# Optimization experiments

Hardware: AMD Instinct MI355X
Metric: run time of the kernel (lower is better)

The kernel has to match this reference:

```python
import jax, jax.numpy as jnp
import numpy as np

D = 256      # n_feature
LVL = 17     # tree depth (leaf levels)
MIX = 20     # M mixture components


def _lstm_cell(x, h, c, Wih, Whh, bih, bhh):
    # torch.nn.LSTMCell gate order: i, f, g, o
    g = x @ Wih.T + bih + h @ Whh.T + bhh
    i, f, gg, o = jnp.split(g, 4, axis=1)
    c2 = jax.nn.sigmoid(f) * c + jax.nn.sigmoid(i) * jnp.tanh(gg)
    return jax.nn.sigmoid(o) * jnp.tanh(c2), c2


def _get_parameter(y, M):
    parts = jnp.split(y[:, :13 * M], 13, axis=1)
    pi = jax.nn.softmax(parts[0], axis=1)
    mu_x, mu_y = parts[1], parts[2]
    sx, sy = jnp.exp(parts[3]), jnp.exp(parts[4])
    rho_xy = jnp.tanh(parts[5])
    mu_a, mu_b = parts[6], parts[7]
    sa, sb = jnp.exp(parts[8]), jnp.exp(parts[9])
    rho_ab = jnp.tanh(parts[10])
    mu_s, ss = parts[11], jnp.exp(parts[12])
    q = jax.nn.softmax(y[:, -3:], axis=1)
    return (pi, mu_x, mu_y, sx, sy, rho_xy, mu_a, mu_b, sa, sb, rho_ab, mu_s, ss, q)


def _bvn_logpdf(dx, dy, mx, my, sx, sy, rho):
    zx = (dx - mx) / sx
    zy = (dy - my) / sy
    Z = zx ** 2 + zy ** 2 - 2.0 * rho * zx * zy
    return -Z / (2.0 * (1.0 - rho ** 2)) - jnp.log(2.0 * jnp.pi * sx * sy * jnp.sqrt(1.0 - rho ** 2))


def _nll(pt, prm):
    # pt: [n, 8] = (x, y, a, b, slope, p1, p2, p3); prm: GMM parameters, each [n, M]
    pi, mx, my, sx, sy, rxy, ma, mb, sa, sb, rab, ms, ss, q = prm
    lpi = jnp.log(pi)
    dx, dy, da, db, ds = (pt[:, k:k + 1] for k in range(5))
    p = pt[:, 5:8]
    lse = jax.scipy.special.logsumexp
    lxy = lse(lpi + _bvn_logpdf(dx, dy, mx, my, sx, sy, rxy), axis=1)
    lab = lse(lpi + _bvn_logpdf(da, db, ma, mb, sa, sb, rab), axis=1)
    lsl = lse(lpi - (ds - ms) ** 2 / (2.0 * ss ** 2) - jnp.log(jnp.sqrt(2.0 * jnp.pi) * ss), axis=1)
    pen = -(p * jnp.log(q)).sum(axis=1)
    return -(lxy + lab + lsl) + pen


def _expected_pos(prm):
    pi, mx, my, sx, sy, rxy, ma, mb, sa, sb, rab, ms, ss, q = prm
    e = lambda m: (pi * m).sum(axis=1)
    return jnp.concatenate([jnp.stack([e(mx), e(my), e(ma), e(mb), e(ms)], axis=1), q], axis=1)


def _levels(I_flat):
    # I_flat is bottom-up concatenation of per-level [ni,3] blocks of a full binary tree
    n_int = I_flat.shape[0]
    L = int(np.log2(n_int + 1))
    sizes = [2 ** (L - 1 - i) for i in range(L)]
    offs = np.concatenate([[0], np.cumsum(sizes)])
    return [I_flat[offs[i]:offs[i + 1]] for i in range(L)]


def setup_inputs() -> dict:
    key = jax.random.key(0)
    ks = jax.random.split(key, 16)
    N = 2 ** (LVL + 1) - 1  # 262143 total nodes
    # heap-layout full binary tree: children of i are 2i+1, 2i+2; bottom-up levels
    blocks = []
    for l in range(LVL - 1, -1, -1):
        f = np.arange(2 ** l - 1, 2 ** (l + 1) - 1)
        blocks.append(np.stack([2 * f + 1, 2 * f + 2, f], axis=1))
    I_flat = jnp.asarray(np.concatenate(blocks, 0), dtype=jnp.int32)
    s = 0.05
    return {
        "X": jax.random.normal(ks[0], (N, 8), jnp.float32),
        "Feature": jax.random.normal(ks[1], (N, D), jnp.float32),
        "I_flat": I_flat,
        "W_ih_e": jax.random.normal(ks[2], (4 * (D // 2), 8), jnp.float32) * s,
        "W_hh_e": jax.random.normal(ks[3], (4 * (D // 2), D // 2), jnp.float32) * s,
        "b_ih_e": jax.random.normal(ks[4], (4 * (D // 2),), jnp.float32) * s,
        "b_hh_e": jax.random.normal(ks[5], (4 * (D // 2),), jnp.float32) * s,
        "fc_h_W": jax.random.normal(ks[6], (2 * D, D), jnp.float32) * s,
        "fc_h_b": jax.random.normal(ks[7], (2 * D,), jnp.float32) * s,
        "W_ih_d": jax.random.normal(ks[8], (4 * D, D + 8), jnp.float32) * s,
        "W_hh_d": jax.random.normal(ks[9], (4 * D, D), jnp.float32) * s,
        "b_ih_d": jax.random.normal(ks[10], (4 * D,), jnp.float32) * s,
        "b_hh_d": jax.random.normal(ks[11], (4 * D,), jnp.float32) * s,
        "fc_W": jax.random.normal(ks[12], (13 * MIX + 3, D // 2), jnp.float32) * s,
        "fc_b": jax.random.normal(ks[13], (13 * MIX + 3,), jnp.float32) * s,
    }


def reference(X, Feature, I_flat, W_ih_e, W_hh_e, b_ih_e, b_hh_e,
              fc_h_W, fc_h_b, W_ih_d, W_hh_d, b_ih_d, b_hh_d, fc_W, fc_b):
    levels = _levels(I_flat)
    num_I = len(levels)

    # ---- encode: bottom-up gather children -> LSTMCell -> scatter father ----
    Feature_New = Feature
    for I in levels:
        li, ri, fi = I[:, 0], I[:, 1], I[:, 2]
        hl, cl = jnp.split(Feature[li], 2, axis=1)
        hr, cr = jnp.split(Feature[ri], 2, axis=1)
        hlo, clo = _lstm_cell(X[li], hl, cl, W_ih_e, W_hh_e, b_ih_e, b_hh_e)
        hro, cro = _lstm_cell(X[ri], hr, cr, W_ih_e, W_hh_e, b_ih_e, b_hh_e)
        out = jnp.concatenate([hlo + hro, clo + cro], axis=1)
        Feature_New = Feature_New.at[fi].set(out)

    # ---- decode: top-down gather father -> LSTMCell+GMM head -> scatter children ----
    X_P = X
    Feat = Feature_New
    Loss = jnp.float32(0.0)
    for I in reversed(levels):
        li, ri, fi = I[:, 0], I[:, 1], I[:, 2]
        p_l, p_r, p_f = X[li], X[ri], X[fi]
        f_f = Feat[fi]
        z = jnp.tanh(f_f @ fc_h_W.T + fc_h_b)
        h_f, c_f = jnp.split(z, 2, axis=1)
        h_o, c_o = _lstm_cell(jnp.concatenate([p_f, f_f], axis=1), h_f, c_f,
                              W_ih_d, W_hh_d, b_ih_d, b_hh_d)
        h_left, h_right = jnp.split(h_o, 2, axis=1)
        c_left, c_right = jnp.split(c_o, 2, axis=1)
        prm_l = _get_parameter(h_left @ fc_W.T + fc_b, MIX)
        prm_r = _get_parameter(h_right @ fc_W.T + fc_b, MIX)
        direct = _nll(p_l, prm_l) + _nll(p_r, prm_r)
        swapped = _nll(p_l, prm_r) + _nll(p_r, prm_l)
        sw = swapped < direct  # l_r_index == 1 -> swap left/right outputs
        Loss = Loss + jnp.mean(jnp.where(sw, swapped, direct))
        pos_l, pos_r = _expected_pos(prm_l), _expected_pos(prm_r)
        feat_l = jnp.concatenate([h_left, c_left], axis=1)
        feat_r = jnp.concatenate([h_right, c_right], axis=1)
        swc = sw[:, None]
        Feat = Feat.at[li].set(jnp.where(swc, feat_r, feat_l))
        Feat = Feat.at[ri].set(jnp.where(swc, feat_l, feat_r))
        X_P = X_P.at[li].set(jnp.where(swc, pos_r, pos_l))
        X_P = X_P.at[ri].set(jnp.where(swc, pos_l, pos_r))
    return Loss / num_I
```

## Files before the change

### kernel.cpp

```cpp
#include <hip/hip_runtime.h>
#include <hip/hip_bf16.h>
#include <math.h>


#define LOG2PI 1.8378770664093453f

typedef __attribute__((ext_vector_type(8))) short short8;
typedef __attribute__((ext_vector_type(4))) float f32x4;

__device__ inline float frcp(float x) { return __builtin_amdgcn_rcpf(x); }
__device__ inline float fexp(float x) { return __expf(x); }
__device__ inline float flog(float x) { return __logf(x); }
__device__ inline float ftanh(float x) {
    float xc = fminf(fmaxf(x, -10.f), 10.f);
    float e = __expf(2.f * xc);
    return (e - 1.f) * frcp(e + 1.f);
}
__device__ inline float sigm(float x) {
    float xc = fminf(fmaxf(x, -30.f), 30.f);
    return frcp(1.f + __expf(-xc));
}

__device__ inline ushort f2b(float v) {
    union { float f; unsigned u; } x; x.f = v;
    unsigned r = x.u + 0x7fffu + ((x.u >> 16) & 1u);
    return (ushort)(r >> 16);
}
__device__ inline float b2f(ushort h) {
    union { unsigned u; float f; } x; x.u = ((unsigned)h) << 16; return x.f;
}

__device__ inline void gload16(const void* g, void* l) {
    __builtin_amdgcn_global_load_lds(
        (const __attribute__((address_space(1))) unsigned*)g,
        (__attribute__((address_space(3))) unsigned*)l, 16, 0, 0);
}

__device__ inline f32x4 mfma16(short8 a, short8 b, f32x4 c) {
    return __builtin_amdgcn_mfma_f32_16x16x32_bf16(a, b, c, 0, 0, 0);
}

__device__ inline float halfmax(float v) {
    #pragma unroll
    for (int o = 16; o >= 1; o >>= 1) v = fmaxf(v, __shfl_xor(v, o));
    return v;
}
__device__ inline float halfsum(float v) {
    #pragma unroll
    for (int o = 16; o >= 1; o >>= 1) v += __shfl_xor(v, o);
    return v;
}
__device__ inline float lse20(float t) {
    float m = halfmax(t);
    float s = halfsum(fexp(t - m));
    return m + flog(s);
}

__device__ inline float nll_node(const ushort* yb, const float* X,
                                 long long fi, int lane, bool& sw_out)
{
    const int half = lane >> 5, k = lane & 31;
    float v = (k < 20) ? b2f(yb[k]) : -INFINITY;
    float mm = halfmax(v);
    float se = halfsum((k < 20) ? fexp(v - mm) : 0.f);
    float lpi = v - mm - flog(se);
    float mx = 0, my = 0, rsx = 1, rsy = 1, rho = 0, hro = 0, cxy = 0;
    float ma = 0, mb2 = 0, rsa = 1, rsb = 1, rab = 0, hra = 0, cab = 0;
    float ms = 0, hrs = 0, csl = 0;
    if (k < 20) {
        mx = b2f(yb[20 + k]); my = b2f(yb[40 + k]);
        float lsx = b2f(yb[60 + k]), lsy = b2f(yb[80 + k]);
        rsx = fexp(-lsx); rsy = fexp(-lsy);
        rho = ftanh(b2f(yb[100 + k]));
        float omr = 1.f - rho * rho;
        hro = 0.5f * frcp(omr);
        cxy = LOG2PI + lsx + lsy + 0.5f * flog(omr);
        ma = b2f(yb[120 + k]); mb2 = b2f(yb[140 + k]);
        float lsa = b2f(yb[160 + k]), lsb = b2f(yb[180 + k]);
        rsa = fexp(-lsa); rsb = fexp(-lsb);
        rab = ftanh(b2f(yb[200 + k]));
        float omr2 = 1.f - rab * rab;
        hra = 0.5f * frcp(omr2);
        cab = LOG2PI + lsa + lsb + 0.5f * flog(omr2);
        ms = b2f(yb[220 + k]); float lss = b2f(yb[240 + k]);
        float rss = fexp(-lss);
        hrs = 0.5f * rss * rss;
        csl = 0.5f * LOG2PI + lss;
    }
    float lq0, lq1, lq2;
    {
        float q0 = b2f(yb[260]), q1 = b2f(yb[261]), q2 = b2f(yb[262]);
        float qm = fmaxf(q0, fmaxf(q1, q2));
        float l = flog(fexp(q0 - qm) + fexp(q1 - qm) + fexp(q2 - qm)) + qm;
        lq0 = q0 - l; lq1 = q1 - l; lq2 = q2 - l;
    }
    const float* pl = X + (size_t)(2 * fi + 1) * 8;
    const float* pr = X + (size_t)(2 * fi + 2) * 8;
    float res[2];
    #pragma unroll
    for (int s = 0; s < 2; ++s) {
        const float* pt = s ? pr : pl;
        float dx = pt[0], dy = pt[1], da = pt[2], db = pt[3], ds = pt[4];
        float t1 = -INFINITY, t2 = -INFINITY, t3 = -INFINITY;
        if (k < 20) {
            float zx = (dx - mx) * rsx, zy = (dy - my) * rsy;
            float Zz = zx * zx + zy * zy - 2.f * rho * zx * zy;
            t1 = lpi - Zz * hro - cxy;
            float za = (da - ma) * rsa, zb = (db - mb2) * rsb;
            float Z2 = za * za + zb * zb - 2.f * rab * za * zb;
            t2 = lpi - Z2 * hra - cab;
            float zs = ds - ms;
            t3 = lpi - zs * zs * hrs - csl;
        }
        float l1 = lse20(t1), l2 = lse20(t2), l3 = lse20(t3);
        float pen = -(pt[5] * lq0 + pt[6] * lq1 + pt[7] * lq2);
        res[s] = -(l1 + l2 + l3) + pen;
    }
    float Aval = half ? res[1] : res[0];
    float Bval = half ? res[0] : res[1];
    float direct = Aval + __shfl_xor(Aval, 32);
    float swapped = Bval + __shfl_xor(Bval, 32);
    sw_out = swapped < direct;
    return sw_out ? swapped : direct;
}

__device__ inline void feat_write_ap(ushort* Ap, const ushort* Hj,
                                     const ushort* Cj, long long fi, bool sw,
                                     int lane)
{
    const size_t rowL = 2 * (size_t)fi + 1;
    const int offL = sw ? 128 : 0;
    const int offR = 128 - offL;
    const int part = lane >> 5;
    const int c = (lane & 31) * 4;
    ushort4 vL = *(const ushort4*)((part ? Cj : Hj) + offL + c);
    ushort4 vR = *(const ushort4*)((part ? Cj : Hj) + offR + c);
    *(ushort4*)(Ap + rowL * 576 + 8 + part * 128 + c) = vL;
    *(ushort4*)(Ap + (rowL + 1) * 576 + 8 + part * 128 + c) = vR;
}

__global__ __launch_bounds__(256) void z_gemm(
    ushort* __restrict__ Apc,
    const ushort* __restrict__ Wz,
    const float* __restrict__ fc_h_b,
    ushort* __restrict__ Zcc,
    int M)
{
    __shared__ ushort As[128 * 64];
    __shared__ ushort Bs[128 * 64];
    const int tid = threadIdx.x;
    const int lane = tid & 63;
    const int w = tid >> 6;
    const int wr = w >> 1, wc = w & 1;
    const int fr = lane & 15, fq = lane >> 4;
    const int m0 = blockIdx.x * 128, n0 = blockIdx.y * 128;

    f32x4 acc[4][4] = {};

    #pragma unroll
    for (int k0 = 0; k0 < 256; k0 += 64) {
        __syncthreads();
        #pragma unroll
        for (int it = 0; it < 4; ++it) {
            const int i = it * 256 + tid;
            const int row = i >> 3, slot = i & 7;
            const int sl = slot ^ (row & 7);
            const int wbase = (i - lane) * 8;
            {
                int gm = m0 + row; gm = gm < M ? gm : M - 1;
                gload16(Apc + (size_t)gm * 576 + 8 + k0 + sl * 8, &As[wbase]);
            }
            {
                int gn = n0 + row; gn = gn < 512 ? gn : 511;
                gload16(Wz + (size_t)gn * 256 + k0 + sl * 8, &Bs[wbase]);
            }
        }
        __syncthreads();
        #pragma unroll
        for (int ks = 0; ks < 2; ++ks) {
            short8 af[4], bfr[4];
            #pragma unroll
            for (int mr = 0; mr < 4; ++mr) {
                const int row = wr * 64 + mr * 16 + fr;
                const int sl = (ks * 4 + fq) ^ (row & 7);
                af[mr] = *(const short8*)&As[row * 64 + sl * 8];
            }
            #pragma unroll
            for (int nc = 0; nc < 4; ++nc) {
                const int row = wc * 64 + nc * 16 + fr;
                const int sl = (ks * 4 + fq) ^ (row & 7);
                bfr[nc] = *(const short8*)&Bs[row * 64 + sl * 8];
            }
            #pragma unroll
            for (int mr = 0; mr < 4; ++mr)
                #pragma unroll
                for (int nc = 0; nc < 4; ++nc)
                    acc[mr][nc] = mfma16(af[mr], bfr[nc], acc[mr][nc]);
        }
    }

    #pragma unroll
    for (int mr = 0; mr < 4; ++mr) {
        #pragma unroll
        for (int j = 0; j < 4; ++j) {
            const int row = m0 + wr * 64 + mr * 16 + fq * 4 + j;
            if (row >= M) continue;
            #pragma unroll
            for (int nc = 0; nc < 4; ++nc) {
                const int col = n0 + wc * 64 + nc * 16 + fr;
                const float z = ftanh(acc[mr][nc][j] + fc_h_b[col]);
                if (col < 256)
                    Apc[(size_t)row * 576 + 264 + col] = f2b(z);
                else
                    Zcc[(size_t)row * 256 + (col - 256)] = f2b(z);
            }
        }
    }
}

__global__ __launch_bounds__(256) void gates_lstm(
    const ushort* __restrict__ Apc,
    const ushort* __restrict__ Wg,
    const float*  __restrict__ bg,
    const ushort* __restrict__ Zcc,
    ushort* __restrict__ H, ushort* __restrict__ C, int M)
{
    __shared__ ushort As[128 * 64];
    __shared__ ushort Bs[128 * 64];
    const int tid = threadIdx.x;
    const int lane = tid & 63;
    const int w = tid >> 6;
    const int wr = w >> 1, wc = w & 1;
    const int fr = lane & 15, fq = lane >> 4;
    const int m0 = blockIdx.x * 128, n0 = blockIdx.y * 128;

    f32x4 acc[4][4] = {};

    #pragma unroll
    for (int k0 = 0; k0 < 576; k0 += 64) {
        __syncthreads();
        #pragma unroll
        for (int it = 0; it < 4; ++it) {
            const int i = it * 256 + tid;
            const int row = i >> 3, slot = i & 7;
            const int sl = slot ^ (row & 7);
            const int wbase = (i - lane) * 8;
            {
                int gm = m0 + row; gm = gm < M ? gm : M - 1;
                gload16(Apc + (size_t)gm * 576 + k0 + sl * 8, &As[wbase]);
            }
            gload16(Wg + (size_t)(n0 + row) * 576 + k0 + sl * 8, &Bs[wbase]);
        }
        __syncthreads();
        #pragma unroll
        for (int ks = 0; ks < 2; ++ks) {
            short8 af[4], bfr[4];
            #pragma unroll
            for (int mr = 0; mr < 4; ++mr) {
                const int row = wr * 64 + mr * 16 + fr;
                const int sl = (ks * 4 + fq) ^ (row & 7);
                af[mr] = *(const short8*)&As[row * 64 + sl * 8];
            }
            #pragma unroll
            for (int nc = 0; nc < 4; ++nc) {
                const int row = wc * 64 + nc * 16 + fr;
                const int sl = (ks * 4 + fq) ^ (row & 7);
                bfr[nc] = *(const short8*)&Bs[row * 64 + sl * 8];
            }
            #pragma unroll
            for (int mr = 0; mr < 4; ++mr)
                #pragma unroll
                for (int nc = 0; nc < 4; ++nc)
                    acc[mr][nc] = mfma16(af[mr], bfr[nc], acc[mr][nc]);
        }
    }

    const int q = fr & 3;
    #pragma unroll
    for (int mr = 0; mr < 4; ++mr) {
        const int node = m0 + wr * 64 + mr * 16 + fq * 4 + q;
        #pragma unroll
        for (int nc = 0; nc < 4; ++nc) {
            const int col = n0 + wc * 64 + nc * 16 + fr;
            f32x4 v = acc[mr][nc];
            const float b = bg[col];
            v[0] += b; v[1] += b; v[2] += b; v[3] += b;
            float gv[4];
            gv[q] = v[q];
            #pragma unroll
            for (int m = 1; m < 4; ++m)
                gv[q ^ m] = __shfl_xor(v[q ^ m], m);
            if (node < M) {
                const int t = (col >> 2) & 255;
                const float cf = b2f(Zcc[(size_t)node * 256 + t]);
                const float c2 = sigm(gv[1]) * cf + sigm(gv[0]) * ftanh(gv[2]);
                const float hv = sigm(gv[3]) * ftanh(c2);
                H[(size_t)node * 256 + t] = f2b(hv);
                C[(size_t)node * 256 + t] = f2b(c2);
            }
        }
    }
}

#define YS 272
__global__ __launch_bounds__(256) void ynll_z(
    const ushort* __restrict__ Hb, const ushort* __restrict__ Cc,
    const ushort* __restrict__ Wyp,
    const float* __restrict__ fc_b, const float* __restrict__ X,
    ushort* __restrict__ Ap,
    const ushort* __restrict__ Wz, const float* __restrict__ fc_h_b,
    ushort* __restrict__ Zcc,
    float* __restrict__ loss,
    int Bc, long long nb_fi, float scale, int writeFeat)
{
    __shared__ char pool[17408] __attribute__((aligned(16)));
    __shared__ float lsum[4];
    ushort* Hs  = (ushort*)pool;
    ushort* Ysb = (ushort*)pool;
    ushort* Fs  = (ushort*)pool;
    const int tid = threadIdx.x;
    const int lane = tid & 63;
    const int wv = tid >> 6;
    const int fr = lane & 15, fq = lane >> 4;
    const int n16 = blockIdx.x * 16;

    #pragma unroll
    for (int it = 0; it < 2; ++it) {
        const int i = it * 256 + tid;
        const int row = i >> 4, slot = i & 15;
        const int sl = slot ^ (row & 7);
        int gr = n16 * 2 + row;
        const int grmax = 2 * Bc - 1;
        gr = gr <= grmax ? gr : grmax;
        gload16(Hb + (size_t)gr * 128 + sl * 8, &Hs[(i - lane) * 8]);
    }
    __syncthreads();

    f32x4 acc[2][5] = {};
    #pragma unroll
    for (int ks = 0; ks < 4; ++ks) {
        short8 a[2];
        #pragma unroll
        for (int rf = 0; rf < 2; ++rf) {
            const int row = rf * 16 + fr;
            const int sl = (ks * 4 + fq) ^ (row & 7);
            a[rf] = *(const short8*)&Hs[row * 128 + sl * 8];
        }
        #pragma unroll
        for (int n = 0; n < 5; ++n) {
            const short8 b = *(const short8*)(
                Wyp + (size_t)(wv * 80 + n * 16 + fr) * 128 + ks * 32 + fq * 8);
            acc[0][n] = mfma16(a[0], b, acc[0][n]);
            acc[1][n] = mfma16(a[1], b, acc[1][n]);
        }
    }
    __syncthreads();

    #pragma unroll
    for (int rf = 0; rf < 2; ++rf)
        #pragma unroll
        for (int n = 0; n < 5; ++n)
            #pragma unroll
            for (int j = 0; j < 4; ++j) {
                const int row = rf * 16 + fq * 4 + j;
                const int col = wv * 80 + n * 16 + fr;
                if (col < 263)
                    Ysb[row * YS + col] = f2b(acc[rf][n][j] + fc_b[col]);
            }
    __syncthreads();

    float wsum = 0.f;
    #pragma unroll
    for (int s4 = 0; s4 < 4; ++s4) {
        const int jj = wv * 4 + s4;
        const int j = n16 + jj;
        if (j >= Bc) break;
        bool sw;
        const long long fi = nb_fi + j;
        wsum += nll_node(&Ysb[(2 * jj + (lane >> 5)) * YS], X, fi, lane, sw);
        if (writeFeat)
            feat_write_ap(Ap, Hb + (size_t)j * 256, Cc + (size_t)j * 256,
                          fi, sw, lane);
    }
    if (lane == 0) lsum[wv] = wsum;
    __syncthreads();
    if (tid == 0)
        atomicAdd(loss, (lsum[0] + lsum[1] + lsum[2] + lsum[3]) * scale);

    if (!writeFeat) return;

    const size_t base = 2 * (size_t)(nb_fi + n16) + 1;
    const int rmax = 2 * Bc - 2 * n16 - 1;
    #pragma unroll
    for (int it = 0; it < 4; ++it) {
        const int i = it * 256 + tid;
        const int row = i >> 5, slot = i & 31;
        const int sl = slot ^ (row & 7);
        int r = row; r = r <= rmax ? r : rmax;
        gload16(Ap + (base + r) * 576 + 8 + sl * 8, &Fs[(i - lane) * 8]);
    }
    __syncthreads();

    f32x4 zacc[2][8] = {};
    for (int ks = 0; ks < 8; ++ks) {
        short8 a[2];
        #pragma unroll
        for (int mf = 0; mf < 2; ++mf) {
            const int r = mf * 16 + fr;
            const int ss = (ks * 4 + fq) ^ (r & 7);
            a[mf] = *(const short8*)&Fs[r * 256 + ss * 8];
        }
        #pragma unroll
        for (int nf = 0; nf < 8; ++nf) {
            const short8 b = *(const short8*)(
                Wz + (size_t)(wv * 128 + nf * 16 + fr) * 256 + ks * 32 + fq * 8);
            zacc[0][nf] = mfma16(a[0], b, zacc[0][nf]);
            zacc[1][nf] = mfma16(a[1], b, zacc[1][nf]);
        }
    }
    #pragma unroll
    for (int mf = 0; mf < 2; ++mf)
        #pragma unroll
        for (int nf = 0; nf < 8; ++nf)
            #pragma unroll
            for (int j = 0; j < 4; ++j) {
                const int r = mf * 16 + fq * 4 + j;
                if (r > rmax) continue;
                const int col = wv * 128 + nf * 16 + fr;
                const float z = ftanh(zacc[mf][nf][j] + fc_h_b[col]);
                if (col < 256)
                    Ap[(base + r) * 576 + 264 + col] = f2b(z);
                else
                    Zcc[(size_t)(2 * n16 + r) * 256 + (col - 256)] = f2b(z);
            }
}

__global__ __launch_bounds__(256) void pack_all(
    const float* __restrict__ fc_h_W, ushort* __restrict__ Wz,
    const float* __restrict__ Wih, const float* __restrict__ Whh,
    ushort* __restrict__ Wg,
    const float* __restrict__ bih, const float* __restrict__ bhh,
    float* __restrict__ bg,
    const float* __restrict__ fcW, ushort* __restrict__ Wy,
    const float* __restrict__ X, ushort* __restrict__ Ap, int nInt)
{
    int i = blockIdx.x * 256 + threadIdx.x;
    if (i < 131072) { Wz[i] = f2b(fc_h_W[i]); return; }
    i -= 131072;
    if (i < 589824) {
        int np = i / 576, c = i - np * 576;
        int n = (np & 3) * 256 + (np >> 2);
        float v = 0.f;
        if (c < 264) v = Wih[n * 264 + c];
        else if (c < 520) v = Whh[n * 256 + (c - 264)];
        Wg[i] = f2b(v);
        return;
    }
    i -= 589824;
    if (i < 1024) {
        int n = (i & 3) * 256 + (i >> 2);
        bg[i] = bih[n] + bhh[n];
        return;
    }
    i -= 1024;
    if (i < 40960) {
        int r = i / 128;
        Wy[i] = f2b(r < 263 ? fcW[i] : 0.f);
        return;
    }
    i -= 40960;
    if (i < nInt * 8) {
        int row = i >> 3, s = i & 7;
        if (s == 0) {
            const float* xs = X + (size_t)row * 8;
            short8 v;
            #pragma unroll
            for (int k = 0; k < 8; ++k)
                ((ushort*)&v)[k] = f2b(xs[k]);
            *(short8*)(Ap + (size_t)row * 576) = v;
        } else {
            short8 z = {0, 0, 0, 0, 0, 0, 0, 0};
            *(short8*)(Ap + (size_t)row * 576 + (64 + s) * 8) = z;
        }
    }
}

__global__ __launch_bounds__(256) void encoder_root(
    const float* __restrict__ X, const float* __restrict__ Feature,
    const float* __restrict__ Wih, const float* __restrict__ Whh,
    const float* __restrict__ bih, const float* __restrict__ bhh,
    ushort* __restrict__ Ap)
{
    __shared__ float gsh[2][512];
    __shared__ float hc[2][256];
    const int t = threadIdx.x;
    for (int ch = 0; ch < 2; ++ch) {
        const int node = 1 + ch;
        const float* x = X + node * 8;
        const float* h = Feature + (size_t)node * 256;
        #pragma unroll
        for (int gi = 0; gi < 2; ++gi) {
            int g = t + gi * 256;
            float s = bih[g] + bhh[g];
            const float* wi = Wih + (size_t)g * 8;
            #pragma unroll
            for (int k = 0; k < 8; ++k) s += wi[k] * x[k];
            const float* wh = Whh + (size_t)g * 128;
            for (int k = 0; k < 128; ++k) s += wh[k] * h[k];
            gsh[ch][g] = s;
        }
    }
    __syncthreads();
    {
        int ch = t >> 7, u = t & 127;
        float i_ = gsh[ch][u], f_ = gsh[ch][128 + u];
        float gg = gsh[ch][256 + u], o_ = gsh[ch][384 + u];
        float c = Feature[(size_t)(1 + ch) * 256 + 128 + u];
        float c2 = sigm(f_) * c + sigm(i_) * ftanh(gg);
        hc[ch][u] = sigm(o_) * ftanh(c2);
        hc[ch][128 + u] = c2;
    }
    __syncthreads();
    Ap[8 + t] = f2b(hc[0][t] + hc[1][t]);
}

extern "C" void kernel_launch(void* const* d_in, const int* in_sizes, int n_in,
                              void* d_out, int out_size, void* d_ws, size_t ws_size,
                              hipStream_t stream)
{
    const float* X       = (const float*)d_in[0];
    const float* Feature = (const float*)d_in[1];
    const float* W_ih_e  = (const float*)d_in[3];
    const float* W_hh_e  = (const float*)d_in[4];
    const float* b_ih_e  = (const float*)d_in[5];
    const float* b_hh_e  = (const float*)d_in[6];
    const float* fc_h_W  = (const float*)d_in[7];
    const float* fc_h_b  = (const float*)d_in[8];
    const float* W_ih_d  = (const float*)d_in[9];
    const float* W_hh_d  = (const float*)d_in[10];
    const float* b_ih_d  = (const float*)d_in[11];
    const float* b_hh_d  = (const float*)d_in[12];
    const float* fc_W    = (const float*)d_in[13];
    const float* fc_b    = (const float*)d_in[14];
    const int Nnodes = in_sizes[0] / 8;
    const int nInt = (Nnodes - 1) / 2;

    float* out = (float*)d_out;
    hipMemsetAsync(d_out, 0, sizeof(float), stream);

    char* cur = (char*)d_ws;
    auto take = [&](size_t bytes) {
        char* p = cur;
        cur += (bytes + 255) & ~(size_t)255;
        return p;
    };
    ushort* Ap  = (ushort*)take((size_t)(nInt + 1) * 576 * 2);
    ushort* Wz  = (ushort*)take((size_t)512 * 256 * 2);
    ushort* Wg  = (ushort*)take((size_t)1024 * 576 * 2);
    ushort* Wy  = (ushort*)take((size_t)320 * 128 * 2);
    float*  bg  = (float*) take((size_t)1024 * 4);
    ushort* Zcc = (ushort*)take((size_t)65536 * 256 * 2);
    ushort* Hb  = (ushort*)take((size_t)65536 * 256 * 2);
    ushort* Cc  = (ushort*)take((size_t)65536 * 256 * 2);

    const int packTotal = 131072 + 589824 + 1024 + 40960 + nInt * 8;
    pack_all<<<(packTotal + 255) / 256, 256, 0, stream>>>(
        fc_h_W, Wz, W_ih_d, W_hh_d, Wg, b_ih_d, b_hh_d, bg, fc_W, Wy,
        X, Ap, nInt);

    encoder_root<<<1, 256, 0, stream>>>(X, Feature, W_ih_e, W_hh_e,
                                        b_ih_e, b_hh_e, Ap);

    z_gemm<<<dim3(1, 4), 256, 0, stream>>>(Ap, Wz, fc_h_b, Zcc, 1);

    for (int l = 0; l < 17; ++l) {
        const int B = 1 << l;
        const long long nb = B - 1;
        const int writeFeat = (l < 16) ? 1 : 0;
        const float scale = 1.f / ((float)B * 17.f);
        const int mg = (B + 127) / 128;
        gates_lstm<<<dim3(mg, 8), 256, 0, stream>>>(
            Ap + (size_t)nb * 576, Wg, bg, Zcc, Hb, Cc, B);
        ynll_z<<<(B + 15) / 16, 256, 0, stream>>>(
            Hb, Cc, Wy, fc_b, X, Ap, Wz, fc_h_b, Zcc, out,
            B, nb, scale, writeFeat);
    }
}
```

Measured before the change: 1.383 ms.

## Split z-projection GEMM out of ynll into a separate per-level z_gemm launch

Removes the fused fc_h projection (Z = tanh(F Wz^T + b)) from the tail of the NLL kernel and instead launches the standalone z_gemm kernel at the start of each level over the level's nodes. The fused version ran a small 32-row MFMA tile per 16-node block, re-reading Wz from global for each block. The standalone GEMM can use larger tiles with better weight reuse. In exchange it adds one kernel launch per level and a global round-trip of the features between kernels.

```diff
diff --git a/kernel.cpp b/kernel.cpp
--- a/kernel.cpp
+++ b/kernel.cpp
@@ -303,21 +303,17 @@
 }
 
 #define YS 272
-__global__ __launch_bounds__(256) void ynll_z(
+__global__ __launch_bounds__(256) void ynll(
     const ushort* __restrict__ Hb, const ushort* __restrict__ Cc,
     const ushort* __restrict__ Wyp,
     const float* __restrict__ fc_b, const float* __restrict__ X,
-    ushort* __restrict__ Ap,
-    const ushort* __restrict__ Wz, const float* __restrict__ fc_h_b,
-    ushort* __restrict__ Zcc,
-    float* __restrict__ loss,
+    ushort* __restrict__ Ap, float* __restrict__ loss,
     int Bc, long long nb_fi, float scale, int writeFeat)
 {
     __shared__ char pool[17408] __attribute__((aligned(16)));
     __shared__ float lsum[4];
     ushort* Hs  = (ushort*)pool;
     ushort* Ysb = (ushort*)pool;
-    ushort* Fs  = (ushort*)pool;
     const int tid = threadIdx.x;
     const int lane = tid & 63;
     const int wv = tid >> 6;
@@ -386,53 +382,6 @@
     __syncthreads();
     if (tid == 0)
         atomicAdd(loss, (lsum[0] + lsum[1] + lsum[2] + lsum[3]) * scale);
-
-    if (!writeFeat) return;
-
-    const size_t base = 2 * (size_t)(nb_fi + n16) + 1;
-    const int rmax = 2 * Bc - 2 * n16 - 1;
-    #pragma unroll
-    for (int it = 0; it < 4; ++it) {
-        const int i = it * 256 + tid;
-        const int row = i >> 5, slot = i & 31;
-        const int sl = slot ^ (row & 7);
-        int r = row; r = r <= rmax ? r : rmax;
-        gload16(Ap + (base + r) * 576 + 8 + sl * 8, &Fs[(i - lane) * 8]);
-    }
-    __syncthreads();
-
-    f32x4 zacc[2][8] = {};
-    for (int ks = 0; ks < 8; ++ks) {
-        short8 a[2];
-        #pragma unroll
-        for (int mf = 0; mf < 2; ++mf) {
-            const int r = mf * 16 + fr;
-            const int ss = (ks * 4 + fq) ^ (r & 7);
-            a[mf] = *(const short8*)&Fs[r * 256 + ss * 8];
-        }
-        #pragma unroll
-        for (int nf = 0; nf < 8; ++nf) {
-            const short8 b = *(const short8*)(
-                Wz + (size_t)(wv * 128 + nf * 16 + fr) * 256 + ks * 32 + fq * 8);
-            zacc[0][nf] = mfma16(a[0], b, zacc[0][nf]);
-            zacc[1][nf] = mfma16(a[1], b, zacc[1][nf]);
-        }
-    }
-    #pragma unroll
-    for (int mf = 0; mf < 2; ++mf)
-        #pragma unroll
-        for (int nf = 0; nf < 8; ++nf)
-            #pragma unroll
-            for (int j = 0; j < 4; ++j) {
-                const int r = mf * 16 + fq * 4 + j;
-                if (r > rmax) continue;
-                const int col = wv * 128 + nf * 16 + fr;
-                const float z = ftanh(zacc[mf][nf][j] + fc_h_b[col]);
-                if (col < 256)
-                    Ap[(base + r) * 576 + 264 + col] = f2b(z);
-                else
-                    Zcc[(size_t)(2 * n16 + r) * 256 + (col - 256)] = f2b(z);
-            }
 }
 
 __global__ __launch_bounds__(256) void pack_all(
@@ -571,18 +520,18 @@
     encoder_root<<<1, 256, 0, stream>>>(X, Feature, W_ih_e, W_hh_e,
                                         b_ih_e, b_hh_e, Ap);
 
-    z_gemm<<<dim3(1, 4), 256, 0, stream>>>(Ap, Wz, fc_h_b, Zcc, 1);
-
     for (int l = 0; l < 17; ++l) {
         const int B = 1 << l;
         const long long nb = B - 1;
         const int writeFeat = (l < 16) ? 1 : 0;
         const float scale = 1.f / ((float)B * 17.f);
         const int mg = (B + 127) / 128;
+        ushort* Apc = Ap + (size_t)nb * 576;
+        z_gemm<<<dim3(mg, 4), 256, 0, stream>>>(Apc, Wz, fc_h_b, Zcc, B);
         gates_lstm<<<dim3(mg, 8), 256, 0, stream>>>(
-            Ap + (size_t)nb * 576, Wg, bg, Zcc, Hb, Cc, B);
-        ynll_z<<<(B + 15) / 16, 256, 0, stream>>>(
-            Hb, Cc, Wy, fc_b, X, Ap, Wz, fc_h_b, Zcc, out,
+            Apc, Wg, bg, Zcc, Hb, Cc, B);
+        ynll<<<(B + 15) / 16, 256, 0, stream>>>(
+            Hb, Cc, Wy, fc_b, X, Ap, out,
             B, nb, scale, writeFeat);
     }
 }
```

Measured after the change: 1.231 ms. -11.0%, faster.

## Split fused NLL/Z kernel at deep levels and source features from H/C

Applied to the files above, without the earlier changes.

The fused NLL+Z kernel is split by tree level. Shallow levels (l<=10) keep a fused variant that reads child features directly from Hb/Cc using swap flags in shared memory, rather than re-reading them from Ap after writing. Deeper levels use a separate NLL kernel followed by a wide z_gemm launch, which gets better parallelism and weight reuse than 16-row blocks. The encoder root computation is folded into block 0 of pack_all to save a launch. The cost is an extra kernel launch per deep level.

```diff
diff --git a/kernel.cpp b/kernel.cpp
--- a/kernel.cpp
+++ b/kernel.cpp
@@ -303,21 +303,17 @@
 }
 
 #define YS 272
-__global__ __launch_bounds__(256) void ynll_z(
+__global__ __launch_bounds__(256) void ynll(
     const ushort* __restrict__ Hb, const ushort* __restrict__ Cc,
     const ushort* __restrict__ Wyp,
     const float* __restrict__ fc_b, const float* __restrict__ X,
-    ushort* __restrict__ Ap,
-    const ushort* __restrict__ Wz, const float* __restrict__ fc_h_b,
-    ushort* __restrict__ Zcc,
-    float* __restrict__ loss,
+    ushort* __restrict__ Ap, float* __restrict__ loss,
     int Bc, long long nb_fi, float scale, int writeFeat)
 {
     __shared__ char pool[17408] __attribute__((aligned(16)));
     __shared__ float lsum[4];
     ushort* Hs  = (ushort*)pool;
     ushort* Ysb = (ushort*)pool;
-    ushort* Fs  = (ushort*)pool;
     const int tid = threadIdx.x;
     const int lane = tid & 63;
     const int wv = tid >> 6;
@@ -386,10 +382,93 @@
     __syncthreads();
     if (tid == 0)
         atomicAdd(loss, (lsum[0] + lsum[1] + lsum[2] + lsum[3]) * scale);
-
-    if (!writeFeat) return;
-
-    const size_t base = 2 * (size_t)(nb_fi + n16) + 1;
+}
+
+__global__ __launch_bounds__(256) void ynll_zs(
+    const ushort* __restrict__ Hb, const ushort* __restrict__ Cc,
+    const ushort* __restrict__ Wyp,
+    const float* __restrict__ fc_b, const float* __restrict__ X,
+    ushort* __restrict__ Ap,
+    const ushort* __restrict__ Wz, const float* __restrict__ fc_h_b,
+    ushort* __restrict__ Zcc,
+    float* __restrict__ loss,
+    int Bc, long long nb_fi, float scale)
+{
+    __shared__ char pool[17408] __attribute__((aligned(16)));
+    __shared__ float lsum[4];
+    __shared__ int sw_sh[16];
+    ushort* Hs  = (ushort*)pool;
+    ushort* Ysb = (ushort*)pool;
+    ushort* Fs  = (ushort*)pool;
+    const int tid = threadIdx.x;
+    const int lane = tid & 63;
+    const int wv = tid >> 6;
+    const int fr = lane & 15, fq = lane >> 4;
+    const int n16 = blockIdx.x * 16;
+
+    #pragma unroll
+    for (int it = 0; it < 2; ++it) {
+        const int i = it * 256 + tid;
+        const int row = i >> 4, slot = i & 15;
+        const int sl = slot ^ (row & 7);
+        int gr = n16 * 2 + row;
+        const int grmax = 2 * Bc - 1;
+        gr = gr <= grmax ? gr : grmax;
+        gload16(Hb + (size_t)gr * 128 + sl * 8, &Hs[(i - lane) * 8]);
+    }
+    __syncthreads();
+
+    f32x4 acc[2][5] = {};
+    #pragma unroll
+    for (int ks = 0; ks < 4; ++ks) {
+        short8 a[2];
+        #pragma unroll
+        for (int rf = 0; rf < 2; ++rf) {
+            const int row = rf * 16 + fr;
+            const int sl = (ks * 4 + fq) ^ (row & 7);
+            a[rf] = *(const short8*)&Hs[row * 128 + sl * 8];
+        }
+        #pragma unroll
+        for (int n = 0; n < 5; ++n) {
+            const short8 b = *(const short8*)(
+                Wyp + (size_t)(wv * 80 + n * 16 + fr) * 128 + ks * 32 + fq * 8);
+            acc[0][n] = mfma16(a[0], b, acc[0][n]);
+            acc[1][n] = mfma16(a[1], b, acc[1][n]);
+        }
+    }
+    __syncthreads();
+
+    #pragma unroll
+    for (int rf = 0; rf < 2; ++rf)
+        #pragma unroll
+        for (int n = 0; n < 5; ++n)
+            #pragma unroll
+            for (int j = 0; j < 4; ++j) {
+                const int row = rf * 16 + fq * 4 + j;
+                const int col = wv * 80 + n * 16 + fr;
+                if (col < 263)
+                    Ysb[row * YS + col] = f2b(acc[rf][n][j] + fc_b[col]);
+            }
+    __syncthreads();
+
+    float wsum = 0.f;
+    #pragma unroll
+    for (int s4 = 0; s4 < 4; ++s4) {
+        const int jj = wv * 4 + s4;
+        const int j = n16 + jj;
+        if (j >= Bc) break;
+        bool sw;
+        const long long fi = nb_fi + j;
+        wsum += nll_node(&Ysb[(2 * jj + (lane >> 5)) * YS], X, fi, lane, sw);
+        if (lane == 0) sw_sh[jj] = sw ? 1 : 0;
+        feat_write_ap(Ap, Hb + (size_t)j * 256, Cc + (size_t)j * 256,
+                      fi, sw, lane);
+    }
+    if (lane == 0) lsum[wv] = wsum;
+    __syncthreads();
+    if (tid == 0)
+        atomicAdd(loss, (lsum[0] + lsum[1] + lsum[2] + lsum[3]) * scale);
+
     const int rmax = 2 * Bc - 2 * n16 - 1;
     #pragma unroll
     for (int it = 0; it < 4; ++it) {
@@ -397,7 +476,14 @@
         const int row = i >> 5, slot = i & 31;
         const int sl = slot ^ (row & 7);
         int r = row; r = r <= rmax ? r : rmax;
-        gload16(Ap + (base + r) * 576 + 8 + sl * 8, &Fs[(i - lane) * 8]);
+        const int pj = r >> 1, side = r & 1;
+        const int sw = sw_sh[pj];
+        const int off = side ? (sw ? 0 : 128) : (sw ? 128 : 0);
+        const int c0 = sl * 8;
+        const ushort* src = (c0 < 128)
+            ? Hb + (size_t)(n16 + pj) * 256 + off + c0
+            : Cc + (size_t)(n16 + pj) * 256 + off + (c0 - 128);
+        gload16(src, &Fs[(i - lane) * 8]);
     }
     __syncthreads();
 
@@ -418,6 +504,7 @@
             zacc[1][nf] = mfma16(a[1], b, zacc[1][nf]);
         }
     }
+    const size_t base = 2 * (size_t)(nb_fi + n16) + 1;
     #pragma unroll
     for (int mf = 0; mf < 2; ++mf)
         #pragma unroll
@@ -442,9 +529,46 @@
     const float* __restrict__ bih, const float* __restrict__ bhh,
     float* __restrict__ bg,
     const float* __restrict__ fcW, ushort* __restrict__ Wy,
-    const float* __restrict__ X, ushort* __restrict__ Ap, int nInt)
-{
-    int i = blockIdx.x * 256 + threadIdx.x;
+    const float* __restrict__ X, ushort* __restrict__ Ap, int nInt,
+    const float* __restrict__ Feature,
+    const float* __restrict__ Wih_e, const float* __restrict__ Whh_e,
+    const float* __restrict__ bih_e, const float* __restrict__ bhh_e)
+{
+    __shared__ float gsh[2][512];
+    __shared__ float hc[2][256];
+    if (blockIdx.x == 0) {
+        const int t = threadIdx.x;
+        for (int ch = 0; ch < 2; ++ch) {
+            const int node = 1 + ch;
+            const float* x = X + node * 8;
+            const float* h = Feature + (size_t)node * 256;
+            #pragma unroll
+            for (int gi = 0; gi < 2; ++gi) {
+                int g = t + gi * 256;
+                float s = bih_e[g] + bhh_e[g];
+                const float* wi = Wih_e + (size_t)g * 8;
+                #pragma unroll
+                for (int k = 0; k < 8; ++k) s += wi[k] * x[k];
+                const float* wh = Whh_e + (size_t)g * 128;
+                for (int k = 0; k < 128; ++k) s += wh[k] * h[k];
+                gsh[ch][g] = s;
+            }
+        }
+        __syncthreads();
+        {
+            int ch = t >> 7, u = t & 127;
+            float i_ = gsh[ch][u], f_ = gsh[ch][128 + u];
+            float gg = gsh[ch][256 + u], o_ = gsh[ch][384 + u];
+            float c = Feature[(size_t)(1 + ch) * 256 + 128 + u];
+            float c2 = sigm(f_) * c + sigm(i_) * ftanh(gg);
+            hc[ch][u] = sigm(o_) * ftanh(c2);
+            hc[ch][128 + u] = c2;
+        }
+        __syncthreads();
+        Ap[8 + t] = f2b(hc[0][t] + hc[1][t]);
+        return;
+    }
+    int i = (blockIdx.x - 1) * 256 + threadIdx.x;
     if (i < 131072) { Wz[i] = f2b(fc_h_W[i]); return; }
     i -= 131072;
     if (i < 589824) {
@@ -483,45 +607,6 @@
             *(short8*)(Ap + (size_t)row * 576 + (64 + s) * 8) = z;
         }
     }
-}
-
-__global__ __launch_bounds__(256) void encoder_root(
-    const float* __restrict__ X, const float* __restrict__ Feature,
-    const float* __restrict__ Wih, const float* __restrict__ Whh,
-    const float* __restrict__ bih, const float* __restrict__ bhh,
-    ushort* __restrict__ Ap)
-{
-    __shared__ float gsh[2][512];
-    __shared__ float hc[2][256];
-    const int t = threadIdx.x;
-    for (int ch = 0; ch < 2; ++ch) {
-        const int node = 1 + ch;
-        const float* x = X + node * 8;
-        const float* h = Feature + (size_t)node * 256;
-        #pragma unroll
-        for (int gi = 0; gi < 2; ++gi) {
-            int g = t + gi * 256;
-            float s = bih[g] + bhh[g];
-            const float* wi = Wih + (size_t)g * 8;
-            #pragma unroll
-            for (int k = 0; k < 8; ++k) s += wi[k] * x[k];
-            const float* wh = Whh + (size_t)g * 128;
-            for (int k = 0; k < 128; ++k) s += wh[k] * h[k];
-            gsh[ch][g] = s;
-        }
-    }
-    __syncthreads();
-    {
-        int ch = t >> 7, u = t & 127;
-        float i_ = gsh[ch][u], f_ = gsh[ch][128 + u];
-        float gg = gsh[ch][256 + u], o_ = gsh[ch][384 + u];
-        float c = Feature[(size_t)(1 + ch) * 256 + 128 + u];
-        float c2 = sigm(f_) * c + sigm(i_) * ftanh(gg);
-        hc[ch][u] = sigm(o_) * ftanh(c2);
-        hc[ch][128 + u] = c2;
-    }
-    __syncthreads();
-    Ap[8 + t] = f2b(hc[0][t] + hc[1][t]);
 }
 
 extern "C" void kernel_launch(void* const* d_in, const int* in_sizes, int n_in,
@@ -564,25 +649,35 @@
     ushort* Cc  = (ushort*)take((size_t)65536 * 256 * 2);
 
     const int packTotal = 131072 + 589824 + 1024 + 40960 + nInt * 8;
-    pack_all<<<(packTotal + 255) / 256, 256, 0, stream>>>(
+    pack_all<<<1 + (packTotal + 255) / 256, 256, 0, stream>>>(
         fc_h_W, Wz, W_ih_d, W_hh_d, Wg, b_ih_d, b_hh_d, bg, fc_W, Wy,
-        X, Ap, nInt);
-
-    encoder_root<<<1, 256, 0, stream>>>(X, Feature, W_ih_e, W_hh_e,
-                                        b_ih_e, b_hh_e, Ap);
+        X, Ap, nInt,
+        Feature, W_ih_e, W_hh_e, b_ih_e, b_hh_e);
 
     z_gemm<<<dim3(1, 4), 256, 0, stream>>>(Ap, Wz, fc_h_b, Zcc, 1);
 
     for (int l = 0; l < 17; ++l) {
         const int B = 1 << l;
         const long long nb = B - 1;
-        const int writeFeat = (l < 16) ? 1 : 0;
         const float scale = 1.f / ((float)B * 17.f);
         const int mg = (B + 127) / 128;
+        ushort* Apc = Ap + (size_t)nb * 576;
         gates_lstm<<<dim3(mg, 8), 256, 0, stream>>>(
-            Ap + (size_t)nb * 576, Wg, bg, Zcc, Hb, Cc, B);
-        ynll_z<<<(B + 15) / 16, 256, 0, stream>>>(
-            Hb, Cc, Wy, fc_b, X, Ap, Wz, fc_h_b, Zcc, out,
-            B, nb, scale, writeFeat);
-    }
-}
+            Apc, Wg, bg, Zcc, Hb, Cc, B);
+        if (l <= 10) {
+            ynll_zs<<<(B + 15) / 16, 256, 0, stream>>>(
+                Hb, Cc, Wy, fc_b, X, Ap, Wz, fc_h_b, Zcc, out,
+                B, nb, scale);
+        } else {
+            const int writeFeat = (l < 16) ? 1 : 0;
+            ynll<<<(B + 15) / 16, 256, 0, stream>>>(
+                Hb, Cc, Wy, fc_b, X, Ap, out,
+                B, nb, scale, writeFeat);
+            if (l < 16) {
+                const int B2 = 2 * B;
+                z_gemm<<<dim3((B2 + 127) / 128, 4), 256, 0, stream>>>(
+                    Ap + (size_t)(2 * B - 1) * 576, Wz, fc_h_b, Zcc, B2);
+            }
+        }
+    }
+}
```

After: 1.292 ms. 1.07x faster.
